# Optimization experiments

Measured on AMD Instinct MI355X. Metric: run time of the kernel, lower is better.

Reference implementation:

```python
import jax, jax.numpy as jnp
import numpy as np

G = 8  # number of shuffle groups (init default)
GN_EPS = 1e-5


def setup_inputs() -> dict:
    key = jax.random.key(0)
    ks = jax.random.split(key, 9)
    C = 512
    cg = C // (2 * G)  # 32: per-branch channel width
    N, H, W = 32, 64, 64
    return {
        "x": jax.random.normal(ks[0], (N, C, H, W), dtype=jnp.float32),
        "cweight": 0.1 * jax.random.normal(ks[1], (1, cg, 1, 1), dtype=jnp.float32),
        "cbias": jnp.ones((1, cg, 1, 1), dtype=jnp.float32),
        "conv1_w": 0.1 * jax.random.normal(ks[2], (cg, cg), dtype=jnp.float32),
        "conv1_b": 0.1 * jax.random.normal(ks[3], (cg,), dtype=jnp.float32),
        "gn_g": jnp.ones((cg,), dtype=jnp.float32),
        "gn_b": jnp.zeros((cg,), dtype=jnp.float32),
        "convh_w": 0.1 * jax.random.normal(ks[4], (cg, cg), dtype=jnp.float32),
        "convh_b": 0.1 * jax.random.normal(ks[5], (cg,), dtype=jnp.float32),
        "convw_w": 0.1 * jax.random.normal(ks[6], (cg, cg), dtype=jnp.float32),
        "convw_b": 0.1 * jax.random.normal(ks[7], (cg,), dtype=jnp.float32),
    }


def _conv1x1(w, b, x):
    # x: [b, ci, h, w] -> [b, co, h, w]
    return jnp.einsum('oi,bihw->bohw', w, x) + b[None, :, None, None]


def _h_swish(y):
    return y * jnp.clip(y + 3.0, 0.0, 6.0) / 6.0


def reference(x, cweight, cbias, conv1_w, conv1_b, gn_g, gn_b,
              convh_w, convh_b, convw_w, convw_b):
    n, c, h, w = x.shape
    xg = x.reshape(n * G, c // G, h, w)          # [nG, 64, h, w]
    x0, x1 = jnp.split(xg, 2, axis=1)            # each [nG, 32, h, w]

    # --- channel attention branch ---
    gap = jnp.mean(x0, axis=(2, 3), keepdims=True)
    x_channel = x0 * jax.nn.sigmoid(cweight * gap + cbias)

    # --- spatial/coordinate attention branch ---
    x_h = jnp.mean(x1, axis=3, keepdims=True)                       # [nG,32,h,1]
    x_w = jnp.mean(x1, axis=2, keepdims=True).transpose(0, 1, 3, 2)  # [nG,32,w,1]
    x_s = jnp.mean(x1, axis=(2, 3), keepdims=True)                  # [nG,32,1,1]

    y = jnp.concatenate([x_h, x_w], axis=2)      # [nG,32,h+w,1]
    y = _conv1x1(conv1_w, conv1_b, y)
    # GroupNorm with groups == channels: per-channel instance norm over spatial dims
    mu = jnp.mean(y, axis=(2, 3), keepdims=True)
    var = jnp.var(y, axis=(2, 3), keepdims=True)
    y = (y - mu) * jax.lax.rsqrt(var + GN_EPS)
    y = y * gn_g[None, :, None, None] + gn_b[None, :, None, None]
    y = _h_swish(y)

    xh, xw = y[:, :, :h, :], y[:, :, h:, :]
    xw = xw.transpose(0, 1, 3, 2)                # [nG,32,1,w]
    a_h = _conv1x1(convh_w, convh_b, xh)         # [nG,32,h,1]
    a_w = _conv1x1(convw_w, convw_b, xw)         # [nG,32,1,w]
    a_hws = a_h * a_w * x_s                      # [nG,32,h,w]
    x_spatial = x1 * jax.nn.sigmoid(a_hws)

    out = jnp.concatenate([x_channel, x_spatial], axis=1)  # [nG,64,h,w]
    out = out.reshape(n, c, h, w)
    # channel shuffle with groups=2
    out = out.reshape(n, 2, c // 2, h, w).transpose(0, 2, 1, 3, 4).reshape(n, c, h, w)
    return out
```

## Files before the change

### kernel.cpp

```cpp
#include <hip/hip_runtime.h>
#include <hip/hip_bf16.h>
#include <math.h>


#define HW 4096
#define CG 32
#define NBG 256

__device__ __forceinline__ float sigmoidf_(float t) {
    return 1.0f / (1.0f + __expf(-t));
}

__global__ __launch_bounds__(64) void k_reduce(
    const float* __restrict__ x,
    const float* __restrict__ cweight, const float* __restrict__ cbias,
    float* __restrict__ s_c, float* __restrict__ x_s,
    float* __restrict__ x_h, float* __restrict__ x_w) {
    int bid = blockIdx.x;
    int bg  = bid >> 6;
    int ch  = bid & 63;
    int b = bg >> 3, g = bg & 7;
    const float4* plane = (const float4*)(x + (size_t)(b * 512 + g * 64 + ch) * HW);
    int l = threadIdx.x;

    __shared__ float rowsum[64];

    float cs0 = 0.f, cs1 = 0.f, cs2 = 0.f, cs3 = 0.f;
#pragma unroll
    for (int i = 0; i < 16; ++i) {
        float4 v = plane[i * 64 + l];
        cs0 += v.x; cs1 += v.y; cs2 += v.z; cs3 += v.w;
        float rs = (v.x + v.y) + (v.z + v.w);
        rs += __shfl_xor(rs, 1);
        rs += __shfl_xor(rs, 2);
        rs += __shfl_xor(rs, 4);
        rs += __shfl_xor(rs, 8);
        if ((l & 15) == 0) rowsum[i * 4 + (l >> 4)] = rs;
    }
    cs0 += __shfl_xor(cs0, 16); cs0 += __shfl_xor(cs0, 32);
    cs1 += __shfl_xor(cs1, 16); cs1 += __shfl_xor(cs1, 32);
    cs2 += __shfl_xor(cs2, 16); cs2 += __shfl_xor(cs2, 32);
    cs3 += __shfl_xor(cs3, 16); cs3 += __shfl_xor(cs3, 32);
    float tot = (cs0 + cs1) + (cs2 + cs3);
    tot += __shfl_xor(tot, 1);
    tot += __shfl_xor(tot, 2);
    tot += __shfl_xor(tot, 4);
    tot += __shfl_xor(tot, 8);

    __syncthreads();

    if (ch < CG) {
        if (l == 0) {
            float gap = tot * (1.0f / HW);
            float t = cweight[ch] * gap + cbias[ch];
            s_c[bg * CG + ch] = sigmoidf_(t);
        }
    } else {
        int c1 = ch - CG;
        if (l == 0) x_s[bg * CG + c1] = tot * (1.0f / HW);
        if (l < 16) {
            float4 cw;
            cw.x = cs0 * (1.0f / 64.0f); cw.y = cs1 * (1.0f / 64.0f);
            cw.z = cs2 * (1.0f / 64.0f); cw.w = cs3 * (1.0f / 64.0f);
            ((float4*)(x_w + (size_t)(bg * CG + c1) * 64))[l] = cw;
        }
        x_h[(size_t)(bg * CG + c1) * 64 + l] = rowsum[l] * (1.0f / 64.0f);
    }
}

__global__ __launch_bounds__(128) void k_mid(
    const float* __restrict__ x_h, const float* __restrict__ x_w,
    const float* __restrict__ x_s,
    const float* __restrict__ w1, const float* __restrict__ b1,
    const float* __restrict__ gn_g, const float* __restrict__ gn_b,
    const float* __restrict__ wh, const float* __restrict__ bh,
    const float* __restrict__ ww, const float* __restrict__ bw,
    float* __restrict__ a_h, float* __restrict__ a_ws) {
    int bg = blockIdx.x;
    int t  = threadIdx.x;

    __shared__ float sv[32][129];
    __shared__ float sy[32][129];
    __shared__ float sw1[32][32], swh[32][32], sww[32][32];
    __shared__ float sb1[32], sbh[32], sbw[32], sgg[32], sgb[32], sxs[32];
    __shared__ float spart[2][4][32];
    __shared__ float sscale[32], sshift[32];

    for (int idx = t; idx < 1024; idx += 128) {
        (&sw1[0][0])[idx] = w1[idx];
        (&swh[0][0])[idx] = wh[idx];
        (&sww[0][0])[idx] = ww[idx];
    }
    if (t < 32) {
        sb1[t] = b1[t]; sbh[t] = bh[t]; sbw[t] = bw[t];
        sgg[t] = gn_g[t]; sgb[t] = gn_b[t];
        sxs[t] = x_s[bg * CG + t];
    }
    for (int i = 0; i < 32; ++i) {
        sv[i][t] = (t < 64) ? x_h[(size_t)(bg * CG + i) * 64 + t]
                            : x_w[(size_t)(bg * CG + i) * 64 + (t - 64)];
    }
    __syncthreads();

    float vloc[32];
#pragma unroll
    for (int i = 0; i < 32; ++i) vloc[i] = sv[i][t];
    for (int o = 0; o < 32; ++o) {
        float acc = sb1[o];
#pragma unroll
        for (int i = 0; i < 32; ++i) acc += sw1[o][i] * vloc[i];
        sy[o][t] = acc;
    }
    __syncthreads();

    {
        int o = t & 31, seg = t >> 5;
        float s = 0.f, ss = 0.f;
#pragma unroll
        for (int p = 0; p < 32; ++p) {
            float v = sy[o][seg * 32 + p];
            s += v; ss += v * v;
        }
        spart[0][seg][o] = s; spart[1][seg][o] = ss;
    }
    __syncthreads();
    if (t < 32) {
        float s  = spart[0][0][t] + spart[0][1][t] + spart[0][2][t] + spart[0][3][t];
        float ss = spart[1][0][t] + spart[1][1][t] + spart[1][2][t] + spart[1][3][t];
        float mu = s * (1.0f / 128.0f);
        float var = ss * (1.0f / 128.0f) - mu * mu;
        float rstd = rsqrtf(var + 1e-5f);
        float sc = rstd * sgg[t];
        sscale[t] = sc;
        sshift[t] = sgb[t] - mu * sc;
    }
    __syncthreads();

    float z[32];
#pragma unroll
    for (int i = 0; i < 32; ++i) {
        float v = sy[i][t] * sscale[i] + sshift[i];
        float c = fminf(fmaxf(v + 3.0f, 0.0f), 6.0f);
        z[i] = v * c * (1.0f / 6.0f);
    }
    if (t < 64) {
        for (int o = 0; o < 32; ++o) {
            float acc = sbh[o];
#pragma unroll
            for (int i = 0; i < 32; ++i) acc += swh[o][i] * z[i];
            a_h[(size_t)(bg * CG + o) * 64 + t] = acc;
        }
    } else {
        int wc = t - 64;
        for (int o = 0; o < 32; ++o) {
            float acc = sbw[o];
#pragma unroll
            for (int i = 0; i < 32; ++i) acc += sww[o][i] * z[i];
            a_ws[(size_t)(bg * CG + o) * 64 + wc] = acc * sxs[o];
        }
    }
}

__global__ __launch_bounds__(256) void k_final(
    const float* __restrict__ x, const float* __restrict__ s_c,
    const float* __restrict__ a_h, const float* __restrict__ a_ws,
    float* __restrict__ out) {
    int bid = blockIdx.x;
    int n  = bid >> 9;
    int cf = bid & 511;
    int j = cf >> 1, k = cf & 1;
    int cc = k * 256 + j;
    int g = cc >> 6, cgi = cc & 63;
    int bg = n * 8 + g;
    const float4* src = (const float4*)(x   + (size_t)(n * 512 + g * 64 + cgi) * HW);
    float4*       dst = (float4*)      (out + (size_t)(n * 512 + cf) * HW);
    int t = threadIdx.x;

    __shared__ float sah[64], saw[64];

    if (cgi < CG) {
        float sc = s_c[bg * CG + cgi];
#pragma unroll
        for (int q = 0; q < 4; ++q) {
            float4 v = src[q * 256 + t];
            v.x *= sc; v.y *= sc; v.z *= sc; v.w *= sc;
            dst[q * 256 + t] = v;
        }
    } else {
        int c1 = cgi - CG;
        if (t < 64)       sah[t]      = a_h [(size_t)(bg * CG + c1) * 64 + t];
        else if (t < 128) saw[t - 64] = a_ws[(size_t)(bg * CG + c1) * 64 + (t - 64)];
        __syncthreads();
#pragma unroll
        for (int q = 0; q < 4; ++q) {
            int vi = q * 256 + t;
            float4 v = src[vi];
            int h  = vi >> 4;
            int wb = (vi & 15) * 4;
            float ah = sah[h];
            v.x *= sigmoidf_(ah * saw[wb + 0]);
            v.y *= sigmoidf_(ah * saw[wb + 1]);
            v.z *= sigmoidf_(ah * saw[wb + 2]);
            v.w *= sigmoidf_(ah * saw[wb + 3]);
            dst[vi] = v;
        }
    }
}

extern "C" void kernel_launch(void* const* d_in, const int* in_sizes, int n_in,
                              void* d_out, int out_size, void* d_ws, size_t ws_size,
                              hipStream_t stream) {
    const float* x        = (const float*)d_in[0];
    const float* cweight  = (const float*)d_in[1];
    const float* cbias    = (const float*)d_in[2];
    const float* conv1_w  = (const float*)d_in[3];
    const float* conv1_b  = (const float*)d_in[4];
    const float* gn_g     = (const float*)d_in[5];
    const float* gn_b     = (const float*)d_in[6];
    const float* convh_w  = (const float*)d_in[7];
    const float* convh_b  = (const float*)d_in[8];
    const float* convw_w  = (const float*)d_in[9];
    const float* convw_b  = (const float*)d_in[10];
    float* out = (float*)d_out;

    float* ws   = (float*)d_ws;
    float* s_c  = ws;
    float* x_s  = s_c  + NBG * CG;
    float* x_h  = x_s  + NBG * CG;
    float* x_w  = x_h  + NBG * CG * 64;
    float* a_h  = x_w  + NBG * CG * 64;
    float* a_ws = a_h  + NBG * CG * 64;

    k_reduce<<<NBG * 64, 64, 0, stream>>>(x, cweight, cbias, s_c, x_s, x_h, x_w);
    k_mid<<<NBG, 128, 0, stream>>>(x_h, x_w, x_s,
                                   conv1_w, conv1_b, gn_g, gn_b,
                                   convh_w, convh_b, convw_w, convw_b,
                                   a_h, a_ws);
    k_final<<<NBG * 64, 256, 0, stream>>>(x, s_c, a_h, a_ws, out);
}
```

Before: 517.6 us.

## Fuse channel-attention output into reduce kernel to avoid re-reading x

The reduce kernel now keeps each plane in registers and, for channel-branch planes, computes the sigmoid gate and writes the shuffled output directly. The final kernel then handles only the spatial-branch half. This removes a second global read of half the input and drops the s_c buffer. Other changes: the reduce kernel is regrouped into 4 waves per block with LDS row-sum partials, and the mid kernel reads weights straight from global memory instead of staging them in shared memory. The trade-off is higher register pressure from holding 16 float4 per lane.

```diff
diff --git a/kernel.cpp b/kernel.cpp
--- a/kernel.cpp
+++ b/kernel.cpp
@@ -11,31 +11,30 @@
     return 1.0f / (1.0f + __expf(-t));
 }
 
-__global__ __launch_bounds__(64) void k_reduce(
+__global__ __launch_bounds__(256) void k_reduce(
     const float* __restrict__ x,
     const float* __restrict__ cweight, const float* __restrict__ cbias,
-    float* __restrict__ s_c, float* __restrict__ x_s,
-    float* __restrict__ x_h, float* __restrict__ x_w) {
-    int bid = blockIdx.x;
-    int bg  = bid >> 6;
-    int ch  = bid & 63;
-    int b = bg >> 3, g = bg & 7;
-    const float4* plane = (const float4*)(x + (size_t)(b * 512 + g * 64 + ch) * HW);
-    int l = threadIdx.x;
-
-    __shared__ float rowsum[64];
+    float* __restrict__ out,
+    float* __restrict__ x_s, float* __restrict__ x_h, float* __restrict__ x_w) {
+    int wid = threadIdx.x >> 6;
+    int l   = threadIdx.x & 63;
+    int gp  = blockIdx.x * 4 + wid;
+    int bg  = gp >> 6;
+    int ch  = gp & 63;
+    int n = bg >> 3, g = bg & 7;
+    const float4* plane = (const float4*)(x + (size_t)(n * 512 + g * 64 + ch) * HW);
+
+    __shared__ float part[4][64][17];
+
+    float4 v[16];
+#pragma unroll
+    for (int i = 0; i < 16; ++i) v[i] = plane[i * 64 + l];
 
     float cs0 = 0.f, cs1 = 0.f, cs2 = 0.f, cs3 = 0.f;
 #pragma unroll
     for (int i = 0; i < 16; ++i) {
-        float4 v = plane[i * 64 + l];
-        cs0 += v.x; cs1 += v.y; cs2 += v.z; cs3 += v.w;
-        float rs = (v.x + v.y) + (v.z + v.w);
-        rs += __shfl_xor(rs, 1);
-        rs += __shfl_xor(rs, 2);
-        rs += __shfl_xor(rs, 4);
-        rs += __shfl_xor(rs, 8);
-        if ((l & 15) == 0) rowsum[i * 4 + (l >> 4)] = rs;
+        cs0 += v[i].x; cs1 += v[i].y; cs2 += v[i].z; cs3 += v[i].w;
+        part[wid][i * 4 + (l >> 4)][l & 15] = (v[i].x + v[i].y) + (v[i].z + v[i].w);
     }
     cs0 += __shfl_xor(cs0, 16); cs0 += __shfl_xor(cs0, 32);
     cs1 += __shfl_xor(cs1, 16); cs1 += __shfl_xor(cs1, 32);
@@ -48,23 +47,31 @@
     tot += __shfl_xor(tot, 8);
 
     __syncthreads();
+    float rsum = 0.f;
+#pragma unroll
+    for (int j = 0; j < 16; ++j) rsum += part[wid][l][j];
 
     if (ch < CG) {
-        if (l == 0) {
-            float gap = tot * (1.0f / HW);
-            float t = cweight[ch] * gap + cbias[ch];
-            s_c[bg * CG + ch] = sigmoidf_(t);
+        float sc = sigmoidf_(cweight[ch] * (tot * (1.0f / HW)) + cbias[ch]);
+        int cc = g * 64 + ch;
+        int cf = 2 * (cc & 255) + (cc >> 8);
+        float4* dst = (float4*)(out + (size_t)(n * 512 + cf) * HW);
+#pragma unroll
+        for (int i = 0; i < 16; ++i) {
+            float4 t = v[i];
+            t.x *= sc; t.y *= sc; t.z *= sc; t.w *= sc;
+            dst[i * 64 + l] = t;
         }
     } else {
         int c1 = ch - CG;
         if (l == 0) x_s[bg * CG + c1] = tot * (1.0f / HW);
+        x_h[(size_t)(bg * CG + c1) * 64 + l] = rsum * (1.0f / 64.0f);
         if (l < 16) {
             float4 cw;
             cw.x = cs0 * (1.0f / 64.0f); cw.y = cs1 * (1.0f / 64.0f);
             cw.z = cs2 * (1.0f / 64.0f); cw.w = cs3 * (1.0f / 64.0f);
             ((float4*)(x_w + (size_t)(bg * CG + c1) * 64))[l] = cw;
         }
-        x_h[(size_t)(bg * CG + c1) * 64 + l] = rowsum[l] * (1.0f / 64.0f);
     }
 }
 
@@ -79,36 +86,21 @@
     int bg = blockIdx.x;
     int t  = threadIdx.x;
 
-    __shared__ float sv[32][129];
     __shared__ float sy[32][129];
-    __shared__ float sw1[32][32], swh[32][32], sww[32][32];
-    __shared__ float sb1[32], sbh[32], sbw[32], sgg[32], sgb[32], sxs[32];
     __shared__ float spart[2][4][32];
     __shared__ float sscale[32], sshift[32];
 
-    for (int idx = t; idx < 1024; idx += 128) {
-        (&sw1[0][0])[idx] = w1[idx];
-        (&swh[0][0])[idx] = wh[idx];
-        (&sww[0][0])[idx] = ww[idx];
-    }
-    if (t < 32) {
-        sb1[t] = b1[t]; sbh[t] = bh[t]; sbw[t] = bw[t];
-        sgg[t] = gn_g[t]; sgb[t] = gn_b[t];
-        sxs[t] = x_s[bg * CG + t];
-    }
+    float vloc[32];
+#pragma unroll
     for (int i = 0; i < 32; ++i) {
-        sv[i][t] = (t < 64) ? x_h[(size_t)(bg * CG + i) * 64 + t]
-                            : x_w[(size_t)(bg * CG + i) * 64 + (t - 64)];
-    }
-    __syncthreads();
-
-    float vloc[32];
-#pragma unroll
-    for (int i = 0; i < 32; ++i) vloc[i] = sv[i][t];
+        vloc[i] = (t < 64) ? x_h[(size_t)(bg * CG + i) * 64 + t]
+                           : x_w[(size_t)(bg * CG + i) * 64 + (t - 64)];
+    }
+
     for (int o = 0; o < 32; ++o) {
-        float acc = sb1[o];
-#pragma unroll
-        for (int i = 0; i < 32; ++i) acc += sw1[o][i] * vloc[i];
+        float acc = b1[o];
+#pragma unroll
+        for (int i = 0; i < 32; ++i) acc += w1[o * 32 + i] * vloc[i];
         sy[o][t] = acc;
     }
     __syncthreads();
@@ -130,9 +122,9 @@
         float mu = s * (1.0f / 128.0f);
         float var = ss * (1.0f / 128.0f) - mu * mu;
         float rstd = rsqrtf(var + 1e-5f);
-        float sc = rstd * sgg[t];
+        float sc = rstd * gn_g[t];
         sscale[t] = sc;
-        sshift[t] = sgb[t] - mu * sc;
+        sshift[t] = gn_b[t] - mu * sc;
     }
     __syncthreads();
 
@@ -145,65 +137,53 @@
     }
     if (t < 64) {
         for (int o = 0; o < 32; ++o) {
-            float acc = sbh[o];
-#pragma unroll
-            for (int i = 0; i < 32; ++i) acc += swh[o][i] * z[i];
+            float acc = bh[o];
+#pragma unroll
+            for (int i = 0; i < 32; ++i) acc += wh[o * 32 + i] * z[i];
             a_h[(size_t)(bg * CG + o) * 64 + t] = acc;
         }
     } else {
         int wc = t - 64;
         for (int o = 0; o < 32; ++o) {
-            float acc = sbw[o];
-#pragma unroll
-            for (int i = 0; i < 32; ++i) acc += sww[o][i] * z[i];
-            a_ws[(size_t)(bg * CG + o) * 64 + wc] = acc * sxs[o];
+            float acc = bw[o];
+#pragma unroll
+            for (int i = 0; i < 32; ++i) acc += ww[o * 32 + i] * z[i];
+            a_ws[(size_t)(bg * CG + o) * 64 + wc] = acc * x_s[bg * CG + o];
         }
     }
 }
 
 __global__ __launch_bounds__(256) void k_final(
-    const float* __restrict__ x, const float* __restrict__ s_c,
+    const float* __restrict__ x,
     const float* __restrict__ a_h, const float* __restrict__ a_ws,
     float* __restrict__ out) {
     int bid = blockIdx.x;
-    int n  = bid >> 9;
-    int cf = bid & 511;
-    int j = cf >> 1, k = cf & 1;
-    int cc = k * 256 + j;
-    int g = cc >> 6, cgi = cc & 63;
-    int bg = n * 8 + g;
-    const float4* src = (const float4*)(x   + (size_t)(n * 512 + g * 64 + cgi) * HW);
+    int bg = bid >> 5;
+    int c1 = bid & 31;
+    int n = bg >> 3, g = bg & 7;
+    int cc = g * 64 + 32 + c1;
+    int cf = 2 * (cc & 255) + (cc >> 8);
+    const float4* src = (const float4*)(x   + (size_t)(n * 512 + g * 64 + 32 + c1) * HW);
     float4*       dst = (float4*)      (out + (size_t)(n * 512 + cf) * HW);
     int t = threadIdx.x;
 
     __shared__ float sah[64], saw[64];
-
-    if (cgi < CG) {
-        float sc = s_c[bg * CG + cgi];
-#pragma unroll
-        for (int q = 0; q < 4; ++q) {
-            float4 v = src[q * 256 + t];
-            v.x *= sc; v.y *= sc; v.z *= sc; v.w *= sc;
-            dst[q * 256 + t] = v;
-        }
-    } else {
-        int c1 = cgi - CG;
-        if (t < 64)       sah[t]      = a_h [(size_t)(bg * CG + c1) * 64 + t];
-        else if (t < 128) saw[t - 64] = a_ws[(size_t)(bg * CG + c1) * 64 + (t - 64)];
-        __syncthreads();
-#pragma unroll
-        for (int q = 0; q < 4; ++q) {
-            int vi = q * 256 + t;
-            float4 v = src[vi];
-            int h  = vi >> 4;
-            int wb = (vi & 15) * 4;
-            float ah = sah[h];
-            v.x *= sigmoidf_(ah * saw[wb + 0]);
-            v.y *= sigmoidf_(ah * saw[wb + 1]);
-            v.z *= sigmoidf_(ah * saw[wb + 2]);
-            v.w *= sigmoidf_(ah * saw[wb + 3]);
-            dst[vi] = v;
-        }
+    if (t < 64)       sah[t]      = a_h [(size_t)(bg * CG + c1) * 64 + t];
+    else if (t < 128) saw[t - 64] = a_ws[(size_t)(bg * CG + c1) * 64 + (t - 64)];
+    __syncthreads();
+
+#pragma unroll
+    for (int q = 0; q < 4; ++q) {
+        int vi = q * 256 + t;
+        float4 v = src[vi];
+        int h  = vi >> 4;
+        int wb = (vi & 15) * 4;
+        float ah = sah[h];
+        v.x *= sigmoidf_(ah * saw[wb + 0]);
+        v.y *= sigmoidf_(ah * saw[wb + 1]);
+        v.z *= sigmoidf_(ah * saw[wb + 2]);
+        v.w *= sigmoidf_(ah * saw[wb + 3]);
+        dst[vi] = v;
     }
 }
 
@@ -224,17 +204,16 @@
     float* out = (float*)d_out;
 
     float* ws   = (float*)d_ws;
-    float* s_c  = ws;
-    float* x_s  = s_c  + NBG * CG;
-    float* x_h  = x_s  + NBG * CG;
-    float* x_w  = x_h  + NBG * CG * 64;
-    float* a_h  = x_w  + NBG * CG * 64;
-    float* a_ws = a_h  + NBG * CG * 64;
-
-    k_reduce<<<NBG * 64, 64, 0, stream>>>(x, cweight, cbias, s_c, x_s, x_h, x_w);
+    float* x_s  = ws;
+    float* x_h  = x_s + NBG * CG;
+    float* x_w  = x_h + NBG * CG * 64;
+    float* a_h  = x_w + NBG * CG * 64;
+    float* a_ws = a_h + NBG * CG * 64;
+
+    k_reduce<<<NBG * 64 / 4, 256, 0, stream>>>(x, cweight, cbias, out, x_s, x_h, x_w);
     k_mid<<<NBG, 128, 0, stream>>>(x_h, x_w, x_s,
                                    conv1_w, conv1_b, gn_g, gn_b,
                                    convh_w, convh_b, convw_w, convw_b,
                                    a_h, a_ws);
-    k_final<<<NBG * 64, 256, 0, stream>>>(x, s_c, a_h, a_ws, out);
-}
+    k_final<<<NBG * CG, 256, 0, stream>>>(x, a_h, a_ws, out);
+}
```

Measured after the change: 507.5 us. About the same (-1.9%).
